# Performance work log

Measured on AMD Instinct MI355X. Metric: run time of the kernel, lower is better.

Reference implementation:

```python
import jax, jax.numpy as jnp
import numpy as np

# ---- static config (from init_kwargs) ----
SCALE = 1.0
N = 16384
DX = SCALE / N          # grid step = cutoff / 2
CUTOFF = 2.0 * DX
SQRT2 = float(np.sqrt(2.0))


def circ_conv(x, w):
    """Circularly-padded 1D cross-correlation (torch Conv1d, padding_mode='circular').
    x: [B, Cin, N], w: [Cout, Cin, K] (K odd). Returns [B, Cout, N]."""
    p = w.shape[-1] // 2
    xp = jnp.concatenate([x[..., -p:], x, x[..., :p]], axis=-1)
    return jax.lax.conv_general_dilated(
        xp, w, window_strides=(1,), padding='VALID',
        dimension_numbers=('NCH', 'OIH', 'NCH'))


def setup_inputs() -> dict:
    key = jax.random.key(0)
    ks = jax.random.split(key, 8)
    x = jax.random.normal(ks[0], (1024, 1, N), dtype=jnp.float32)
    # centered 4th-order accurate first-derivative stencil (acc=4), scaled by 1/dx
    deriv = np.array([1.0 / 12.0, -2.0 / 3.0, 0.0, 2.0 / 3.0, -1.0 / 12.0],
                     dtype=np.float32) / DX
    deriv_w = jnp.asarray(deriv).reshape(1, 1, 5)
    # discrete Box filter of width cutoff = 2*dx (trapezoidal weights)
    filt_w = jnp.asarray(np.array([0.25, 0.5, 0.25], dtype=np.float32)).reshape(1, 1, 3)
    # BasicNet(in=2, mid=[6,3], out=1, k=5, bias=True): kaiming-ish scaled init
    def conv_init(k, cout, cin, ks_):
        return jax.random.normal(k, (cout, cin, ks_), dtype=jnp.float32) / np.sqrt(cin * ks_)
    W1 = conv_init(ks[1], 6, 2, 5); b1 = jax.random.normal(ks[2], (6,), dtype=jnp.float32) * 0.01
    W2 = conv_init(ks[3], 3, 6, 5); b2 = jax.random.normal(ks[4], (3,), dtype=jnp.float32) * 0.01
    W3 = conv_init(ks[5], 1, 3, 5); b3 = jax.random.normal(ks[6], (1,), dtype=jnp.float32) * 0.01
    return {"x": x, "deriv_w": deriv_w, "filt_w": filt_w,
            "W1": W1, "b1": b1, "W2": W2, "b2": b2, "W3": W3, "b3": b3}


def reference(x, deriv_w, filt_w, W1, b1, W2, b2, W3, b3):
    xdiff = circ_conv(x, deriv_w)                                # [B,1,N]
    feat = jnp.concatenate([xdiff, x - circ_conv(x, filt_w)], axis=1)  # [B,2,N]
    h = jax.nn.elu(circ_conv(feat, W1) + b1[None, :, None])      # [B,6,N]
    h = jax.nn.elu(circ_conv(h, W2) + b2[None, :, None])         # [B,3,N]
    cs = jax.nn.elu(circ_conv(h, W3) + b3[None, :, None])        # [B,1,N]
    cs = jnp.clip(cs, 0.0, 1.0)                                  # Hardtanh(bounds)
    y = (cs * CUTOFF) ** 2 * jnp.abs(xdiff) * xdiff
    return circ_conv(SQRT2 * y, deriv_w)
```

## Files before the change

kernel.cpp:

```cpp
#include <hip/hip_runtime.h>
#include <math.h>

#define NN 16384
#define T 512

typedef float f2 __attribute__((ext_vector_type(2)));

__device__ __forceinline__ f2 elu2(f2 v) {
    f2 e;
    e.x = __expf(v.x);
    e.y = __expf(v.y);
    const f2 zero = (f2)0.0f;
    return __builtin_elementwise_max(v, zero)
         + __builtin_elementwise_min(e - 1.0f, zero);
}

__global__ void smag_setup(const float* __restrict__ dw,
                           const float* __restrict__ fw,
                           const float* __restrict__ W1,
                           float* __restrict__ cw)
{
    const int t = threadIdx.x;
    if (t < 54) {
        const int c = t / 9;
        const int m = (t % 9) - 4;
        float acc = 0.0f;
        #pragma unroll
        for (int k = 0; k < 5; ++k) {
            int j = m + 4 - k;
            if (j >= 0 && j <= 4) acc += W1[c * 10 + k] * dw[j];
        }
        if (m >= -2 && m <= 2) acc += W1[c * 10 + 5 + (m + 2)];
        #pragma unroll
        for (int i = 0; i < 3; ++i) {
            int k = m + 3 - i;
            if (k >= 0 && k <= 4) acc -= fw[i] * W1[c * 10 + 5 + k];
        }
        cw[t] = acc;
    }
}

__global__ __launch_bounds__(256, 8)
void smag_c9(const float* __restrict__ x,
             const float* __restrict__ dw,
             const float* __restrict__ cw,
             const float* __restrict__ b1,
             const float* __restrict__ W2, const float* __restrict__ b2,
             const float* __restrict__ W3, const float* __restrict__ b3,
             float* __restrict__ out)
{
    const int blk = blockIdx.x & 31;
    const int row = blockIdx.x >> 5;
    const int tb  = blk * T;
    const int tid = threadIdx.x;
    const float* __restrict__ xr = x   + (size_t)row * NN;
    float* __restrict__ outr     = out + (size_t)row * NN;

    __shared__ __align__(16) float sm[4704];
    float* const sh1 = sm;
    float* const sy  = sm;
    float* const sh2 = sm + 3144;

    const float d0 = dw[0], d1 = dw[1], d2 = dw[2], d3 = dw[3], d4 = dw[4];

    f2 xd_main, xd_tail;
    auto S2p = [&](int p, f2& xd_out) {
        f2 G[6];
        #pragma unroll
        for (int t = 0; t < 6; ++t) {
            int g = (tb + p - 4 + 2 * t + NN) & (NN - 1);
            G[t] = *(const f2*)(xr + g);
        }
        f2 w9[9] = {G[0], {G[0].y, G[1].x}, G[1], {G[1].y, G[2].x}, G[2],
                    {G[2].y, G[3].x}, G[3], {G[3].y, G[4].x}, G[4]};
        #pragma unroll
        for (int c = 0; c < 6; ++c) {
            f2 a = (f2)b1[c];
            #pragma unroll
            for (int m = 0; m < 9; ++m)
                a = a + w9[m] * cw[c * 9 + m];
            *(f2*)(sh1 + c * 524 + p + 6) = elu2(a);
        }
        f2 a12 = {G[3].y, G[4].x};
        f2 a34 = {G[4].y, G[5].x};
        xd_out = G[3] * d0 + a12 * d1 + G[4] * d2 + a34 * d3 + G[5] * d4;
    };
    S2p(2 * tid - 6, xd_main);
    if (tid < 6) S2p(506 + 2 * tid, xd_tail);
    __syncthreads();

    auto S3 = [&](int q) {
        f2 acc0 = (f2)b2[0], acc1 = (f2)b2[1], acc2 = (f2)b2[2];
        #pragma unroll
        for (int ci = 0; ci < 6; ++ci) {
            const float* hb = sh1 + ci * 524 + q + 4;
            f2 H0 = *(f2*)(hb);
            f2 H1 = *(f2*)(hb + 2);
            f2 H2 = *(f2*)(hb + 4);
            f2 ha[5] = {H0, {H0.y, H1.x}, H1, {H1.y, H2.x}, H2};
            #pragma unroll
            for (int k = 0; k < 5; ++k) {
                acc0 = acc0 + ha[k] * W2[0 * 30 + ci * 5 + k];
                acc1 = acc1 + ha[k] * W2[1 * 30 + ci * 5 + k];
                acc2 = acc2 + ha[k] * W2[2 * 30 + ci * 5 + k];
            }
        }
        *(f2*)(sh2 + 0 * 520 + q + 4) = elu2(acc0);
        *(f2*)(sh2 + 1 * 520 + q + 4) = elu2(acc1);
        *(f2*)(sh2 + 2 * 520 + q + 4) = elu2(acc2);
    };
    S3(2 * tid - 4);
    if (tid < 4) S3(508 + 2 * tid);
    __syncthreads();

    const float B3v = b3[0];
    const float K = 1.41421356237309515f * (float)(2.0/16384.0) * (float)(2.0/16384.0);
    auto S4 = [&](int q, f2 xd) {
        f2 a = (f2)B3v;
        #pragma unroll
        for (int ci = 0; ci < 3; ++ci) {
            const float* hb = sh2 + ci * 520 + q + 2;
            f2 H0 = *(f2*)(hb);
            f2 H1 = *(f2*)(hb + 2);
            f2 H2 = *(f2*)(hb + 4);
            f2 ha1 = {H0.y, H1.x};
            f2 ha3 = {H1.y, H2.x};
            a = a + H0 * W3[ci * 5 + 0] + ha1 * W3[ci * 5 + 1] + H1 * W3[ci * 5 + 2]
                  + ha3 * W3[ci * 5 + 3] + H2 * W3[ci * 5 + 4];
        }
        f2 cs = __builtin_elementwise_min(__builtin_elementwise_max(a, (f2)0.0f), (f2)1.0f);
        f2 axd = __builtin_elementwise_abs(xd);
        f2 y = (cs * cs) * (axd * xd) * K;
        *(f2*)(sy + q + 2) = y;
    };
    S4(2 * tid - 2, xd_main);
    if (tid < 2) S4(510 + 2 * tid, xd_tail);
    __syncthreads();

    {
        const int p = 2 * tid;
        f2 Y0 = *(f2*)(sy + p);
        f2 Y1 = *(f2*)(sy + p + 2);
        f2 Y2 = *(f2*)(sy + p + 4);
        f2 a12 = {Y0.y, Y1.x};
        f2 a34 = {Y1.y, Y2.x};
        f2 o = Y0 * d0 + a12 * d1 + Y1 * d2 + a34 * d3 + Y2 * d4;
        *(f2*)(outr + tb + p) = o;
    }
}

extern "C" void kernel_launch(void* const* d_in, const int* in_sizes, int n_in,
                              void* d_out, int out_size, void* d_ws, size_t ws_size,
                              hipStream_t stream) {
    const float* x  = (const float*)d_in[0];
    const float* dw = (const float*)d_in[1];
    const float* fw = (const float*)d_in[2];
    const float* W1 = (const float*)d_in[3];
    const float* b1 = (const float*)d_in[4];
    const float* W2 = (const float*)d_in[5];
    const float* b2 = (const float*)d_in[6];
    const float* W3 = (const float*)d_in[7];
    const float* b3 = (const float*)d_in[8];
    float* out = (float*)d_out;
    float* cw  = (float*)d_ws;

    hipLaunchKernelGGL(smag_setup, dim3(1), dim3(64), 0, stream, dw, fw, W1, cw);

    const int B = 1024;
    dim3 grid(B * (NN / T));
    dim3 block(256);
    hipLaunchKernelGGL(smag_c9, grid, block, 0, stream,
                       x, dw, cw, b1, W2, b2, W3, b3, out);
}
```

Baseline: 111.5 us.

## Compute four outputs per thread with 128-thread blocks and float4 LDS access

Each thread now produces four consecutive outputs per stage instead of two, and the block shrinks from 256 to 128 threads to cover the same 512-point tile. Overlapping stencil windows share loaded global and shared-memory values, and shared-memory reads and writes use float4 vectors. This cuts load and instruction overhead per output. In exchange it raises register pressure, lowers the occupancy hint from 8 to 4 waves, and the smaller halo branches now run on fewer threads.

```diff
diff --git a/kernel.cpp b/kernel.cpp
--- a/kernel.cpp
+++ b/kernel.cpp
@@ -5,6 +5,7 @@
 #define T 512
 
 typedef float f2 __attribute__((ext_vector_type(2)));
+typedef float f4 __attribute__((ext_vector_type(4)));
 
 __device__ __forceinline__ f2 elu2(f2 v) {
     f2 e;
@@ -40,8 +41,8 @@
     }
 }
 
-__global__ __launch_bounds__(256, 8)
-void smag_c9(const float* __restrict__ x,
+__global__ __launch_bounds__(128, 4)
+void smag_q4(const float* __restrict__ x,
              const float* __restrict__ dw,
              const float* __restrict__ cw,
              const float* __restrict__ b1,
@@ -63,89 +64,105 @@
 
     const float d0 = dw[0], d1 = dw[1], d2 = dw[2], d3 = dw[3], d4 = dw[4];
 
-    f2 xd_main, xd_tail;
-    auto S2p = [&](int p, f2& xd_out) {
-        f2 G[6];
+    f2 xd0_m, xd1_m, xd0_t, xd1_t;
+    auto S2p = [&](int p, f2& xd0, f2& xd1) {
+        f2 G[7];
         #pragma unroll
-        for (int t = 0; t < 6; ++t) {
-            int g = (tb + p - 4 + 2 * t + NN) & (NN - 1);
-            G[t] = *(const f2*)(xr + g);
+        for (int i = 0; i < 7; ++i) {
+            int g = (tb + p - 4 + 2 * i + NN) & (NN - 1);
+            G[i] = *(const f2*)(xr + g);
         }
-        f2 w9[9] = {G[0], {G[0].y, G[1].x}, G[1], {G[1].y, G[2].x}, G[2],
-                    {G[2].y, G[3].x}, G[3], {G[3].y, G[4].x}, G[4]};
+        f2 o[6];
+        #pragma unroll
+        for (int i = 0; i < 6; ++i) o[i] = (f2){G[i].y, G[i + 1].x};
         #pragma unroll
         for (int c = 0; c < 6; ++c) {
-            f2 a = (f2)b1[c];
+            const float* w = cw + c * 9;
+            f2 a0 = (f2)b1[c];
+            f2 a1 = a0;
             #pragma unroll
-            for (int m = 0; m < 9; ++m)
-                a = a + w9[m] * cw[c * 9 + m];
-            *(f2*)(sh1 + c * 524 + p + 6) = elu2(a);
+            for (int k = 0; k < 5; ++k) {
+                a0 = a0 + G[k] * w[2 * k];
+                a1 = a1 + G[k + 1] * w[2 * k];
+            }
+            #pragma unroll
+            for (int k = 0; k < 4; ++k) {
+                a0 = a0 + o[k] * w[2 * k + 1];
+                a1 = a1 + o[k + 1] * w[2 * k + 1];
+            }
+            f2 e0 = elu2(a0), e1 = elu2(a1);
+            *(f4*)(sh1 + c * 524 + p + 6) = (f4){e0.x, e0.y, e1.x, e1.y};
         }
-        f2 a12 = {G[3].y, G[4].x};
-        f2 a34 = {G[4].y, G[5].x};
-        xd_out = G[3] * d0 + a12 * d1 + G[4] * d2 + a34 * d3 + G[5] * d4;
+        xd0 = G[3] * d0 + o[3] * d1 + G[4] * d2 + o[4] * d3 + G[5] * d4;
+        xd1 = G[4] * d0 + o[4] * d1 + G[5] * d2 + o[5] * d3 + G[6] * d4;
     };
-    S2p(2 * tid - 6, xd_main);
-    if (tid < 6) S2p(506 + 2 * tid, xd_tail);
+    S2p(4 * tid - 6, xd0_m, xd1_m);
+    if (tid < 3) S2p(506 + 4 * tid, xd0_t, xd1_t);
     __syncthreads();
 
     auto S3 = [&](int q) {
-        f2 acc0 = (f2)b2[0], acc1 = (f2)b2[1], acc2 = (f2)b2[2];
+        f2 ac0[3], ac1[3];
+        #pragma unroll
+        for (int oc = 0; oc < 3; ++oc) { ac0[oc] = (f2)b2[oc]; ac1[oc] = ac0[oc]; }
         #pragma unroll
         for (int ci = 0; ci < 6; ++ci) {
             const float* hb = sh1 + ci * 524 + q + 4;
-            f2 H0 = *(f2*)(hb);
-            f2 H1 = *(f2*)(hb + 2);
-            f2 H2 = *(f2*)(hb + 4);
-            f2 ha[5] = {H0, {H0.y, H1.x}, H1, {H1.y, H2.x}, H2};
+            f4 A = *(const f4*)(hb);
+            f4 B = *(const f4*)(hb + 4);
+            f2 w0 = {A.x, A.y}, w1 = {A.y, A.z}, w2 = {A.z, A.w};
+            f2 w3 = {A.w, B.x}, w4 = {B.x, B.y}, w5 = {B.y, B.z}, w6 = {B.z, B.w};
             #pragma unroll
-            for (int k = 0; k < 5; ++k) {
-                acc0 = acc0 + ha[k] * W2[0 * 30 + ci * 5 + k];
-                acc1 = acc1 + ha[k] * W2[1 * 30 + ci * 5 + k];
-                acc2 = acc2 + ha[k] * W2[2 * 30 + ci * 5 + k];
+            for (int oc = 0; oc < 3; ++oc) {
+                const float* ww = W2 + oc * 30 + ci * 5;
+                ac0[oc] = ac0[oc] + w0 * ww[0] + w1 * ww[1] + w2 * ww[2] + w3 * ww[3] + w4 * ww[4];
+                ac1[oc] = ac1[oc] + w2 * ww[0] + w3 * ww[1] + w4 * ww[2] + w5 * ww[3] + w6 * ww[4];
             }
         }
-        *(f2*)(sh2 + 0 * 520 + q + 4) = elu2(acc0);
-        *(f2*)(sh2 + 1 * 520 + q + 4) = elu2(acc1);
-        *(f2*)(sh2 + 2 * 520 + q + 4) = elu2(acc2);
+        #pragma unroll
+        for (int oc = 0; oc < 3; ++oc) {
+            f2 e0 = elu2(ac0[oc]), e1 = elu2(ac1[oc]);
+            *(f4*)(sh2 + oc * 520 + q + 4) = (f4){e0.x, e0.y, e1.x, e1.y};
+        }
     };
-    S3(2 * tid - 4);
-    if (tid < 4) S3(508 + 2 * tid);
+    S3(4 * tid - 4);
+    if (tid < 2) S3(508 + 4 * tid);
     __syncthreads();
 
     const float B3v = b3[0];
     const float K = 1.41421356237309515f * (float)(2.0/16384.0) * (float)(2.0/16384.0);
-    auto S4 = [&](int q, f2 xd) {
-        f2 a = (f2)B3v;
+    auto S4 = [&](int q, f2 xd0, f2 xd1) {
+        f2 a0 = (f2)B3v, a1 = a0;
         #pragma unroll
         for (int ci = 0; ci < 3; ++ci) {
             const float* hb = sh2 + ci * 520 + q + 2;
-            f2 H0 = *(f2*)(hb);
-            f2 H1 = *(f2*)(hb + 2);
-            f2 H2 = *(f2*)(hb + 4);
-            f2 ha1 = {H0.y, H1.x};
-            f2 ha3 = {H1.y, H2.x};
-            a = a + H0 * W3[ci * 5 + 0] + ha1 * W3[ci * 5 + 1] + H1 * W3[ci * 5 + 2]
-                  + ha3 * W3[ci * 5 + 3] + H2 * W3[ci * 5 + 4];
+            f4 A = *(const f4*)(hb);
+            f4 B = *(const f4*)(hb + 4);
+            f2 w0 = {A.x, A.y}, w1 = {A.y, A.z}, w2 = {A.z, A.w};
+            f2 w3 = {A.w, B.x}, w4 = {B.x, B.y}, w5 = {B.y, B.z}, w6 = {B.z, B.w};
+            const float* ww = W3 + ci * 5;
+            a0 = a0 + w0 * ww[0] + w1 * ww[1] + w2 * ww[2] + w3 * ww[3] + w4 * ww[4];
+            a1 = a1 + w2 * ww[0] + w3 * ww[1] + w4 * ww[2] + w5 * ww[3] + w6 * ww[4];
         }
-        f2 cs = __builtin_elementwise_min(__builtin_elementwise_max(a, (f2)0.0f), (f2)1.0f);
-        f2 axd = __builtin_elementwise_abs(xd);
-        f2 y = (cs * cs) * (axd * xd) * K;
-        *(f2*)(sy + q + 2) = y;
+        const f2 zero = (f2)0.0f, one = (f2)1.0f;
+        f2 c0 = __builtin_elementwise_min(__builtin_elementwise_max(a0, zero), one);
+        f2 c1 = __builtin_elementwise_min(__builtin_elementwise_max(a1, zero), one);
+        f2 y0 = (c0 * c0) * (__builtin_elementwise_abs(xd0) * xd0) * K;
+        f2 y1 = (c1 * c1) * (__builtin_elementwise_abs(xd1) * xd1) * K;
+        *(f4*)(sy + q + 2) = (f4){y0.x, y0.y, y1.x, y1.y};
     };
-    S4(2 * tid - 2, xd_main);
-    if (tid < 2) S4(510 + 2 * tid, xd_tail);
+    S4(4 * tid - 2, xd0_m, xd1_m);
+    if (tid < 1) S4(510 + 4 * tid, xd0_t, xd1_t);
     __syncthreads();
 
     {
-        const int p = 2 * tid;
-        f2 Y0 = *(f2*)(sy + p);
-        f2 Y1 = *(f2*)(sy + p + 2);
-        f2 Y2 = *(f2*)(sy + p + 4);
-        f2 a12 = {Y0.y, Y1.x};
-        f2 a34 = {Y1.y, Y2.x};
-        f2 o = Y0 * d0 + a12 * d1 + Y1 * d2 + a34 * d3 + Y2 * d4;
-        *(f2*)(outr + tb + p) = o;
+        const int p = 4 * tid;
+        f4 A = *(const f4*)(sy + p);
+        f4 B = *(const f4*)(sy + p + 4);
+        f2 w0 = {A.x, A.y}, w1 = {A.y, A.z}, w2 = {A.z, A.w};
+        f2 w3 = {A.w, B.x}, w4 = {B.x, B.y}, w5 = {B.y, B.z}, w6 = {B.z, B.w};
+        f2 o0 = w0 * d0 + w1 * d1 + w2 * d2 + w3 * d3 + w4 * d4;
+        f2 o1 = w2 * d0 + w3 * d1 + w4 * d2 + w5 * d3 + w6 * d4;
+        *(f4*)(outr + tb + p) = (f4){o0.x, o0.y, o1.x, o1.y};
     }
 }
 
@@ -168,7 +185,7 @@
 
     const int B = 1024;
     dim3 grid(B * (NN / T));
-    dim3 block(256);
-    hipLaunchKernelGGL(smag_c9, grid, block, 0, stream,
+    dim3 block(128);
+    hipLaunchKernelGGL(smag_q4, grid, block, 0, stream,
                        x, dw, cw, b1, W2, b2, W3, b3, out);
 }
```

New measurement: 130.0 us. 16.6% more time.
